# Optimization experiments

Hardware: AMD Instinct MI355X
Metric: run time of the kernel (lower is better)

The kernel has to match this reference:

```python
import jax, jax.numpy as jnp
import numpy as np


def setup_inputs() -> dict:
    key = jax.random.key(0)
    k1, k2 = jax.random.split(key)
    a_bar = jax.random.normal(k1, (32, 512, 512), dtype=jnp.float32)
    b_bar = jax.random.normal(k2, (32, 512, 512), dtype=jnp.float32)
    return {"a_bar": a_bar, "b_bar": b_bar}


def reference(a_bar, b_bar):
    # e[b,i,j] = <a_bar[b,i,:], b_bar[b,j,:]>
    e = jnp.einsum("bid,bjd->bij", a_bar, b_bar)
    # a_tilde: row softmax (over j) then weighted sum of b rows
    attn_a = jax.nn.softmax(e, axis=2)            # [B, Sa, Sb]
    a_tilde = jnp.einsum("bij,bjd->bid", attn_a, b_bar)
    # b_tilde: column softmax (over i), transposed, times a_bar
    attn_b = jax.nn.softmax(e, axis=1)            # [B, Sa, Sb]
    b_tilde = jnp.einsum("bij,bid->bjd", attn_b, a_bar)
    m_a = jnp.concatenate([a_bar, a_tilde, a_bar - a_tilde, a_bar * a_tilde], axis=-1)
    m_b = jnp.concatenate([b_bar, b_tilde, b_bar - b_tilde, b_bar * b_tilde], axis=-1)
    return (m_a, m_b)
```

## Files before the change

### kernel.cpp

```cpp
#include <hip/hip_runtime.h>
#include <hip/hip_bf16.h>
#include <math.h>

#define B_   32
#define S_   512
#define SxS  (S_ * S_)
#define LOG2E 1.4426950408889634f

using frag_ab = __attribute__((ext_vector_type(8))) short;
using frag_cd = __attribute__((ext_vector_type(4))) float;

__device__ inline short f2bf(float x) {
    __hip_bfloat16 h = __float2bfloat16(x);
    return *reinterpret_cast<short*>(&h);
}
__device__ inline float bf2f(short s) {
    __hip_bfloat16 h = *reinterpret_cast<__hip_bfloat16*>(&s);
    return __bfloat162float(h);
}
__device__ __forceinline__ int swz(int r) { return (r ^ (r >> 3)) & 7; }

__device__ __forceinline__ void async16(const short* g, short* l) {
    __builtin_amdgcn_global_load_lds(
        (const __attribute__((address_space(1))) void*)g,
        (__attribute__((address_space(3))) void*)l,
        16, 0, 0);
}

__global__ __launch_bounds__(256) void k_prep(const float* __restrict__ A,
                                              const float* __restrict__ Bm,
                                              short* __restrict__ PA,
                                              short* __restrict__ PB,
                                              short* __restrict__ Va,
                                              short* __restrict__ Vb)
{
    const int z   = blockIdx.z;
    const int b   = z & 31;
    const int isB = z >> 5;
    const float* X = (isB ? Bm : A) + (size_t)b * SxS;
    short* P  = (isB ? PB : PA) + (size_t)b * (S_ * 1024);
    short* Vp = (isB ? Vb : Va) + (size_t)b * SxS;
    const float scale = isB ? 1.0f : LOG2E;

    const int i0 = blockIdx.y * 64, d0 = blockIdx.x * 64;

    __shared__ short T[64][72];

    const int sl = threadIdx.x & 7;
    const int il = threadIdx.x >> 3;

    #pragma unroll
    for (int p = 0; p < 2; ++p) {
        const int i    = il + 32 * p;
        const int rowg = i0 + i;
        const float* src = X + (size_t)rowg * S_ + d0 + sl * 8;
        const float4 v0 = *(const float4*)(src);
        const float4 v1 = *(const float4*)(src + 4);

        T[sl * 8 + 0][i] = f2bf(v0.x); T[sl * 8 + 1][i] = f2bf(v0.y);
        T[sl * 8 + 2][i] = f2bf(v0.z); T[sl * 8 + 3][i] = f2bf(v0.w);
        T[sl * 8 + 4][i] = f2bf(v1.x); T[sl * 8 + 5][i] = f2bf(v1.y);
        T[sl * 8 + 6][i] = f2bf(v1.z); T[sl * 8 + 7][i] = f2bf(v1.w);

        const float xs[8] = {v0.x, v0.y, v0.z, v0.w, v1.x, v1.y, v1.z, v1.w};
        frag_ab hi, lo;
        #pragma unroll
        for (int j = 0; j < 8; ++j) {
            const float x = xs[j] * scale;
            const short h = f2bf(x);
            hi[j] = h;
            lo[j] = f2bf(x - bf2f(h));
        }
        const int W = (d0 >> 5) + (sl >> 2);
        const int q = sl & 3;
        short* base = P + (size_t)rowg * 1024 + W * 64;
        *(frag_ab*)(base + (((2 * q)     ^ (rowg & 7)) * 8)) = hi;
        *(frag_ab*)(base + (((2 * q + 1) ^ (rowg & 7)) * 8)) = lo;
    }
    __syncthreads();

    const int pc = threadIdx.x & 7, dl = threadIdx.x >> 3;
    #pragma unroll
    for (int p = 0; p < 2; ++p) {
        const int d  = dl + 32 * p;
        const int dg = d0 + d;
        frag_ab t = *(const frag_ab*)&T[d][pc * 8];
        *(frag_ab*)(Vp + (size_t)dg * 512 + i0 + ((pc ^ (dg & 7)) * 8)) = t;
    }
}

__global__ __launch_bounds__(256) void k_gemm_e(const short* __restrict__ PA,
                                                const short* __restrict__ PB,
                                                float* __restrict__ E)
{
    const int lin     = blockIdx.x + (blockIdx.y << 2) + (blockIdx.z << 4);
    const int logical = ((lin & 7) << 6) + (lin >> 3);
    const int b  = logical >> 4;
    const int i0 = ((logical >> 2) & 3) * 128;
    const int j0 = (logical & 3) * 128;

    const short* Ab = PA + (size_t)b * (S_ * 1024);
    const short* Bb = PB + (size_t)b * (S_ * 1024);
    float* Eb = E + (size_t)b * SxS;

    __shared__ __align__(16) short As[128][64];
    __shared__ __align__(16) short Bs[128][64];

    const int tid  = threadIdx.x;
    const int wave = tid >> 6, lane = tid & 63;
    const int wr   = wave >> 1, wc = wave & 1;
    const int q    = lane >> 4, m = lane & 15;
    const int srow = lane >> 3, schunk = lane & 7;

    frag_cd zero = {0.f, 0.f, 0.f, 0.f};
    frag_cd acc[4][4];
    #pragma unroll
    for (int i = 0; i < 4; ++i)
        #pragma unroll
        for (int j = 0; j < 4; ++j) acc[i][j] = zero;

    for (int k0 = 0; k0 < S_; k0 += 32) {
        const int W = k0 >> 5;
        __syncthreads();
        #pragma unroll
        for (int p = 0; p < 4; ++p) {
            const int seg    = wave * 4 + p;
            const int rowg_a = i0 + seg * 8 + srow;
            const int rowg_b = j0 + seg * 8 + srow;
            async16(Ab + (size_t)rowg_a * 1024 + W * 64 + schunk * 8, &As[seg * 8][0]);
            async16(Bb + (size_t)rowg_b * 1024 + W * 64 + schunk * 8, &Bs[seg * 8][0]);
        }
        __syncthreads();

        frag_ab ah[4], al[4], bh[4], bl[4];
        #pragma unroll
        for (int t = 0; t < 4; ++t) {
            const int ra = wr * 64 + t * 16 + m;
            const int rb = wc * 64 + t * 16 + m;
            ah[t] = *(const frag_ab*)&As[ra][((2 * q)     ^ (ra & 7)) * 8];
            al[t] = *(const frag_ab*)&As[ra][((2 * q + 1) ^ (ra & 7)) * 8];
            bh[t] = *(const frag_ab*)&Bs[rb][((2 * q)     ^ (rb & 7)) * 8];
            bl[t] = *(const frag_ab*)&Bs[rb][((2 * q + 1) ^ (rb & 7)) * 8];
        }
        #pragma unroll
        for (int mt = 0; mt < 4; ++mt)
            #pragma unroll
            for (int nt = 0; nt < 4; ++nt) {
                acc[mt][nt] = __builtin_amdgcn_mfma_f32_16x16x32_bf16(ah[mt], bh[nt], acc[mt][nt], 0, 0, 0);
                acc[mt][nt] = __builtin_amdgcn_mfma_f32_16x16x32_bf16(ah[mt], bl[nt], acc[mt][nt], 0, 0, 0);
                acc[mt][nt] = __builtin_amdgcn_mfma_f32_16x16x32_bf16(al[mt], bh[nt], acc[mt][nt], 0, 0, 0);
            }
    }

    #pragma unroll
    for (int mt = 0; mt < 4; ++mt)
        #pragma unroll
        for (int nt = 0; nt < 4; ++nt) {
            const int rb  = i0 + wr * 64 + mt * 16 + q * 4;
            const int col = j0 + wc * 64 + nt * 16 + m;
            Eb[(size_t)(rb + 0) * S_ + col] = acc[mt][nt][0];
            Eb[(size_t)(rb + 1) * S_ + col] = acc[mt][nt][1];
            Eb[(size_t)(rb + 2) * S_ + col] = acc[mt][nt][2];
            Eb[(size_t)(rb + 3) * S_ + col] = acc[mt][nt][3];
        }
}

__global__ __launch_bounds__(256) void k_rstats(const float* __restrict__ E,
                                                float* __restrict__ rmax,
                                                float* __restrict__ rinv)
{
    const int row  = blockIdx.x * 4 + (threadIdx.x >> 6);
    const int lane = threadIdx.x & 63;
    const float* er = E + (size_t)row * S_;

    float4 v0 = *(const float4*)(er + lane * 4);
    float4 v1 = *(const float4*)(er + 256 + lane * 4);

    float m = fmaxf(fmaxf(fmaxf(v0.x, v0.y), fmaxf(v0.z, v0.w)),
                    fmaxf(fmaxf(v1.x, v1.y), fmaxf(v1.z, v1.w)));
    #pragma unroll
    for (int off = 32; off >= 1; off >>= 1)
        m = fmaxf(m, __shfl_xor(m, off));

    float s = exp2f(v0.x - m) + exp2f(v0.y - m)
            + exp2f(v0.z - m) + exp2f(v0.w - m)
            + exp2f(v1.x - m) + exp2f(v1.y - m)
            + exp2f(v1.z - m) + exp2f(v1.w - m);
    #pragma unroll
    for (int off = 32; off >= 1; off >>= 1)
        s += __shfl_xor(s, off);

    if (lane == 0) { rmax[row] = m; rinv[row] = 1.0f / s; }
}

__global__ __launch_bounds__(256) void k_cstats(const float* __restrict__ E,
                                                float* __restrict__ cmax,
                                                float* __restrict__ cinv)
{
    const int b  = blockIdx.x >> 3;
    const int s0 = (blockIdx.x & 7) * 64;
    const float* Eb = E + (size_t)b * SxS;

    __shared__ float scr[32][64];
    __shared__ float mS[64];

    const int tid = threadIdx.x;
    const int ib  = tid >> 3;
    const int sub = tid & 7;

    float pm[8];
    #pragma unroll
    for (int c = 0; c < 8; ++c) pm[c] = -INFINITY;
    for (int ii = 0; ii < 16; ++ii) {
        const float* p = Eb + (size_t)(ib * 16 + ii) * S_ + s0 + sub * 8;
        const float4 u  = *(const float4*)p;
        const float4 u2 = *(const float4*)(p + 4);
        pm[0] = fmaxf(pm[0], u.x);  pm[1] = fmaxf(pm[1], u.y);
        pm[2] = fmaxf(pm[2], u.z);  pm[3] = fmaxf(pm[3], u.w);
        pm[4] = fmaxf(pm[4], u2.x); pm[5] = fmaxf(pm[5], u2.y);
        pm[6] = fmaxf(pm[6], u2.z); pm[7] = fmaxf(pm[7], u2.w);
    }
    #pragma unroll
    for (int c = 0; c < 8; ++c) scr[ib][sub * 8 + c] = pm[c];
    __syncthreads();
    if (tid < 64) {
        float v = scr[0][tid];
        #pragma unroll
        for (int k = 1; k < 32; ++k) v = fmaxf(v, scr[k][tid]);
        mS[tid] = v;
        cmax[b * S_ + s0 + tid] = v;
    }
    __syncthreads();

    float ps[8];
    #pragma unroll
    for (int c = 0; c < 8; ++c) ps[c] = 0.f;
    for (int ii = 0; ii < 16; ++ii) {
        const float* p = Eb + (size_t)(ib * 16 + ii) * S_ + s0 + sub * 8;
        const float4 u  = *(const float4*)p;
        const float4 u2 = *(const float4*)(p + 4);
        const float xs[8] = {u.x, u.y, u.z, u.w, u2.x, u2.y, u2.z, u2.w};
        #pragma unroll
        for (int c = 0; c < 8; ++c) ps[c] += exp2f(xs[c] - mS[sub * 8 + c]);
    }
    __syncthreads();
    #pragma unroll
    for (int c = 0; c < 8; ++c) scr[ib][sub * 8 + c] = ps[c];
    __syncthreads();
    if (tid < 64) {
        float v = 0.f;
        #pragma unroll
        for (int k = 0; k < 32; ++k) v += scr[k][tid];
        cinv[b * S_ + s0 + tid] = 1.0f / v;
    }
}

__global__ __launch_bounds__(256) void k_pv(const float* __restrict__ E,
                                            const float* __restrict__ rmx_,
                                            const float* __restrict__ rin_,
                                            const float* __restrict__ cmx_,
                                            const float* __restrict__ cin_,
                                            const short* __restrict__ Va,
                                            const short* __restrict__ Vb,
                                            const float* __restrict__ A,
                                            const float* __restrict__ Bm,
                                            float* __restrict__ Ma,
                                            float* __restrict__ Mb)
{
    const int lin = blockIdx.x;
    const int wg  = ((lin & 7) << 8) | (lin >> 3);
    const int side = wg >> 10;
    const int b    = (wg >> 5) & 31;
    const int rs   = (wg >> 1) & 15;
    const int dh   = wg & 1;
    const int s0   = rs * 32;

    const float* Eb  = E + (size_t)b * SxS;
    const float* pmx = (side ? cmx_ : rmx_) + b * S_;
    const float* piv = (side ? cin_ : rin_) + b * S_;
    const short* Vg  = (side ? Va : Vb) + (size_t)b * SxS;
    const float* Xb  = (side ? Bm : A) + (size_t)b * SxS;
    float* Ob = (side ? Mb : Ma) + (size_t)b * S_ * 2048;

    __shared__ __align__(16) short Pl[32][512];
    __shared__ __align__(16) short Vs[256][64];
    __shared__ float riS[32];

    const int tid = threadIdx.x;
    const int wv  = tid >> 6, lane = tid & 63;
    const int q   = lane >> 4, m = lane & 15;

    if (tid < 32) riS[tid] = piv[s0 + tid];

    if (side == 0) {
        const int rl = tid >> 3, sub = tid & 7;
        const float mx = pmx[s0 + rl];
        const float* er = Eb + (size_t)(s0 + rl) * S_;
        const int sl = (sub ^ swz(rl)) * 8;
        #pragma unroll
        for (int fi = 0; fi < 8; ++fi) {
            const float* p = er + sub * 8 + fi * 64;
            const float4 u  = *(const float4*)p;
            const float4 u2 = *(const float4*)(p + 4);
            const float xs[8] = {u.x, u.y, u.z, u.w, u2.x, u2.y, u2.z, u2.w};
            frag_ab pb;
            #pragma unroll
            for (int j = 0; j < 8; ++j) pb[j] = f2bf(exp2f(xs[j] - mx));
            *(frag_ab*)&Pl[rl][fi * 64 + sl] = pb;
        }
    } else {
        const int ib = tid >> 2, cs = tid & 3;
        float mloc[8];
        #pragma unroll
        for (int c = 0; c < 8; ++c) mloc[c] = pmx[s0 + cs * 8 + c];
        frag_ab pb[8];
        #pragma unroll
        for (int ii = 0; ii < 8; ++ii) {
            const float* p = Eb + (size_t)(ib * 8 + ii) * S_ + s0 + cs * 8;
            const float4 u  = *(const float4*)p;
            const float4 u2 = *(const float4*)(p + 4);
            const float xs[8] = {u.x, u.y, u.z, u.w, u2.x, u2.y, u2.z, u2.w};
            #pragma unroll
            for (int c = 0; c < 8; ++c)
                pb[c][ii] = f2bf(exp2f(xs[c] - mloc[c]));
        }
        #pragma unroll
        for (int c = 0; c < 8; ++c) {
            const int cl = cs * 8 + c;
            *(frag_ab*)&Pl[cl][((ib ^ swz(cl)) & 63) * 8
                               + (ib & ~7) * 0] = pb[c];
        }
    }

    frag_cd zero = {0.f, 0.f, 0.f, 0.f};
    frag_cd acc[2][4];
    #pragma unroll
    for (int i = 0; i < 2; ++i)
        #pragma unroll
        for (int j = 0; j < 4; ++j) acc[i][j] = zero;

    for (int k0 = 0; k0 < S_; k0 += 64) {
        __syncthreads();
        #pragma unroll
        for (int p = 0; p < 8; ++p) {
            const int seg = p * 32 + wv * 8;
            const int d   = dh * 256 + seg + (lane >> 3);
            async16(Vg + (size_t)d * 512 + k0 + (lane & 7) * 8, &Vs[seg][0]);
        }
        __syncthreads();

        #pragma unroll
        for (int kk = 0; kk < 2; ++kk) {
            frag_ab af[2], bf[4];
            #pragma unroll
            for (int t = 0; t < 2; ++t) {
                const int ra = t * 16 + m;
                af[t] = *(const frag_ab*)&Pl[ra][k0 + (((kk * 4 + q) ^ swz(ra)) * 8)];
            }
            #pragma unroll
            for (int t = 0; t < 4; ++t) {
                const int dl = wv * 64 + t * 16 + m;
                bf[t] = *(const frag_ab*)&Vs[dl][(((kk * 4 + q) ^ (dl & 7)) * 8)];
            }
            #pragma unroll
            for (int mt = 0; mt < 2; ++mt)
                #pragma unroll
                for (int nt = 0; nt < 4; ++nt)
                    acc[mt][nt] = __builtin_amdgcn_mfma_f32_16x16x32_bf16(af[mt], bf[nt], acc[mt][nt], 0, 0, 0);
        }
    }

    #pragma unroll
    for (int mt = 0; mt < 2; ++mt)
        #pragma unroll
        for (int nt = 0; nt < 4; ++nt) {
            const int colg = dh * 256 + wv * 64 + nt * 16 + m;
            #pragma unroll
            for (int rr = 0; rr < 4; ++rr) {
                const int rl   = mt * 16 + q * 4 + rr;
                const int rowg = s0 + rl;
                const float at = acc[mt][nt][rr] * riS[rl];
                const float xv = Xb[(size_t)rowg * S_ + colg];
                float* o = Ob + (size_t)rowg * 2048 + colg;
                o[0]    = xv;
                o[512]  = at;
                o[1024] = xv - at;
                o[1536] = xv * at;
            }
        }
}

extern "C" void kernel_launch(void* const* d_in, const int* in_sizes, int n_in,
                              void* d_out, int out_size, void* d_ws, size_t ws_size,
                              hipStream_t stream)
{
    const float* A  = (const float*)d_in[0];
    const float* Bm = (const float*)d_in[1];
    float* Ma = (float*)d_out;
    float* Mb = Ma + (size_t)B_ * S_ * 2048;

    float* E    = (float*)d_ws;
    short* Va   = (short*)(E + (size_t)B_ * SxS);
    short* Vb   = Va + (size_t)B_ * SxS;
    float* rmax = (float*)(Vb + (size_t)B_ * SxS);
    float* rinv = rmax + B_ * S_;
    float* cmax = rinv + B_ * S_;
    float* cinv = cmax + B_ * S_;

    short* PA = (short*)d_out;
    short* PB = PA + (size_t)B_ * S_ * 1024;

    k_prep  <<<dim3(8, 8, 64),    256, 0, stream>>>(A, Bm, PA, PB, Va, Vb);
    k_gemm_e<<<dim3(4, 4, 32),    256, 0, stream>>>(PA, PB, E);
    k_rstats<<<dim3(B_ * S_ / 4), 256, 0, stream>>>(E, rmax, rinv);
    k_cstats<<<dim3(B_ * 8),      256, 0, stream>>>(E, cmax, cinv);
    k_pv    <<<dim3(2048),        256, 0, stream>>>(E, rmax, rinv, cmax, cinv,
                                                    Va, Vb, A, Bm, Ma, Mb);
}
```

Baseline: 475.7 us.

## Fuse five-kernel pipeline into one cooperative persistent kernel with grid syncs

Replaces the five separate launches (prep, E GEMM, row stats, column stats, PV) with a single cooperative kernel of 256 persistent blocks that loops over the original work items and separates the phases with grid.sync(). The aim is to remove per-launch overhead and inter-kernel gaps. The cost is that each phase now runs on only 256 workgroups with about 64KB of shared memory each, which lowers occupancy and parallelism, especially in the E GEMM phase, which has only 512 tiles. If the cooperative launch fails, it falls back to the old launches.

Result: slower. 615.5 us (+29.4%).

```diff
diff --git a/kernel.cpp b/kernel.cpp
--- a/kernel.cpp
+++ b/kernel.cpp
@@ -1,6 +1,9 @@
 #include <hip/hip_runtime.h>
+#include <hip/hip_cooperative_groups.h>
 #include <hip/hip_bf16.h>
 #include <math.h>
+
+namespace cg = cooperative_groups;
 
 #define B_   32
 #define S_   512
@@ -25,6 +28,371 @@
         (const __attribute__((address_space(1))) void*)g,
         (__attribute__((address_space(3))) void*)l,
         16, 0, 0);
+}
+
+__global__ __launch_bounds__(256) void k_mega(const float* __restrict__ A,
+                                              const float* __restrict__ Bm,
+                                              short* __restrict__ PA,
+                                              short* __restrict__ PB,
+                                              short* __restrict__ Va,
+                                              short* __restrict__ Vb,
+                                              float* __restrict__ E,
+                                              float* __restrict__ rmax,
+                                              float* __restrict__ rinv,
+                                              float* __restrict__ cmax,
+                                              float* __restrict__ cinv,
+                                              float* __restrict__ Ma,
+                                              float* __restrict__ Mb)
+{
+    cg::grid_group grid = cg::this_grid();
+    const int pb  = blockIdx.x;
+    const int tid = threadIdx.x;
+
+    __shared__ __align__(16) char smem[65792];
+
+    {
+        short (*T)[72] = (short(*)[72])smem;
+        const int sl = tid & 7;
+        const int il = tid >> 3;
+        const int pc = tid & 7, dl = tid >> 3;
+
+        for (int lin = pb; lin < 4096; lin += 256) {
+            __syncthreads();
+            const int bx = lin & 7, by = (lin >> 3) & 7, z = lin >> 6;
+            const int b   = z & 31;
+            const int isB = z >> 5;
+            const float* X = (isB ? Bm : A) + (size_t)b * SxS;
+            short* P  = (isB ? PB : PA) + (size_t)b * (S_ * 1024);
+            short* Vp = (isB ? Vb : Va) + (size_t)b * SxS;
+            const float scale = isB ? 1.0f : LOG2E;
+            const int i0 = by * 64, d0 = bx * 64;
+
+            #pragma unroll
+            for (int pp = 0; pp < 2; ++pp) {
+                const int i    = il + 32 * pp;
+                const int rowg = i0 + i;
+                const float* src = X + (size_t)rowg * S_ + d0 + sl * 8;
+                const float4 v0 = *(const float4*)(src);
+                const float4 v1 = *(const float4*)(src + 4);
+
+                T[sl * 8 + 0][i] = f2bf(v0.x); T[sl * 8 + 1][i] = f2bf(v0.y);
+                T[sl * 8 + 2][i] = f2bf(v0.z); T[sl * 8 + 3][i] = f2bf(v0.w);
+                T[sl * 8 + 4][i] = f2bf(v1.x); T[sl * 8 + 5][i] = f2bf(v1.y);
+                T[sl * 8 + 6][i] = f2bf(v1.z); T[sl * 8 + 7][i] = f2bf(v1.w);
+
+                const float xs[8] = {v0.x, v0.y, v0.z, v0.w, v1.x, v1.y, v1.z, v1.w};
+                frag_ab hi, lo;
+                #pragma unroll
+                for (int j = 0; j < 8; ++j) {
+                    const float x = xs[j] * scale;
+                    const short h = f2bf(x);
+                    hi[j] = h;
+                    lo[j] = f2bf(x - bf2f(h));
+                }
+                const int W = (d0 >> 5) + (sl >> 2);
+                const int q = sl & 3;
+                short* base = P + (size_t)rowg * 1024 + W * 64;
+                *(frag_ab*)(base + (((2 * q)     ^ (rowg & 7)) * 8)) = hi;
+                *(frag_ab*)(base + (((2 * q + 1) ^ (rowg & 7)) * 8)) = lo;
+            }
+            __syncthreads();
+
+            #pragma unroll
+            for (int pp = 0; pp < 2; ++pp) {
+                const int d  = dl + 32 * pp;
+                const int dg = d0 + d;
+                frag_ab t = *(const frag_ab*)&T[d][pc * 8];
+                *(frag_ab*)(Vp + (size_t)dg * 512 + i0 + ((pc ^ (dg & 7)) * 8)) = t;
+            }
+        }
+    }
+    __syncthreads();
+    grid.sync();
+
+    {
+        short (*As)[64] = (short(*)[64])smem;
+        short (*Bs)[64] = (short(*)[64])(smem + 16384);
+
+        const int wave = tid >> 6, lane = tid & 63;
+        const int wr   = wave >> 1, wc = wave & 1;
+        const int q    = lane >> 4, m = lane & 15;
+        const int srow = lane >> 3, schunk = lane & 7;
+
+        for (int lin = pb; lin < 512; lin += 256) {
+            const int logical = ((lin & 7) << 6) + (lin >> 3);
+            const int b  = logical >> 4;
+            const int i0 = ((logical >> 2) & 3) * 128;
+            const int j0 = (logical & 3) * 128;
+
+            const short* Ab = PA + (size_t)b * (S_ * 1024);
+            const short* Bb = PB + (size_t)b * (S_ * 1024);
+            float* Eb = E + (size_t)b * SxS;
+
+            frag_cd zero = {0.f, 0.f, 0.f, 0.f};
+            frag_cd acc[4][4];
+            #pragma unroll
+            for (int i = 0; i < 4; ++i)
+                #pragma unroll
+                for (int j = 0; j < 4; ++j) acc[i][j] = zero;
+
+            for (int k0 = 0; k0 < S_; k0 += 32) {
+                const int W = k0 >> 5;
+                __syncthreads();
+                #pragma unroll
+                for (int p = 0; p < 4; ++p) {
+                    const int seg    = wave * 4 + p;
+                    const int rowg_a = i0 + seg * 8 + srow;
+                    const int rowg_b = j0 + seg * 8 + srow;
+                    async16(Ab + (size_t)rowg_a * 1024 + W * 64 + schunk * 8, &As[seg * 8][0]);
+                    async16(Bb + (size_t)rowg_b * 1024 + W * 64 + schunk * 8, &Bs[seg * 8][0]);
+                }
+                __syncthreads();
+
+                frag_ab ah[4], al[4], bh[4], bl[4];
+                #pragma unroll
+                for (int t = 0; t < 4; ++t) {
+                    const int ra = wr * 64 + t * 16 + m;
+                    const int rb = wc * 64 + t * 16 + m;
+                    ah[t] = *(const frag_ab*)&As[ra][((2 * q)     ^ (ra & 7)) * 8];
+                    al[t] = *(const frag_ab*)&As[ra][((2 * q + 1) ^ (ra & 7)) * 8];
+                    bh[t] = *(const frag_ab*)&Bs[rb][((2 * q)     ^ (rb & 7)) * 8];
+                    bl[t] = *(const frag_ab*)&Bs[rb][((2 * q + 1) ^ (rb & 7)) * 8];
+                }
+                #pragma unroll
+                for (int mt = 0; mt < 4; ++mt)
+                    #pragma unroll
+                    for (int nt = 0; nt < 4; ++nt) {
+                        acc[mt][nt] = __builtin_amdgcn_mfma_f32_16x16x32_bf16(ah[mt], bh[nt], acc[mt][nt], 0, 0, 0);
+                        acc[mt][nt] = __builtin_amdgcn_mfma_f32_16x16x32_bf16(ah[mt], bl[nt], acc[mt][nt], 0, 0, 0);
+                        acc[mt][nt] = __builtin_amdgcn_mfma_f32_16x16x32_bf16(al[mt], bh[nt], acc[mt][nt], 0, 0, 0);
+                    }
+            }
+
+            #pragma unroll
+            for (int mt = 0; mt < 4; ++mt)
+                #pragma unroll
+                for (int nt = 0; nt < 4; ++nt) {
+                    const int rb  = i0 + wr * 64 + mt * 16 + q * 4;
+                    const int col = j0 + wc * 64 + nt * 16 + m;
+                    Eb[(size_t)(rb + 0) * S_ + col] = acc[mt][nt][0];
+                    Eb[(size_t)(rb + 1) * S_ + col] = acc[mt][nt][1];
+                    Eb[(size_t)(rb + 2) * S_ + col] = acc[mt][nt][2];
+                    Eb[(size_t)(rb + 3) * S_ + col] = acc[mt][nt][3];
+                }
+            __syncthreads();
+        }
+    }
+    grid.sync();
+
+    {
+        const int lane = tid & 63;
+        for (int lin = pb; lin < 4096; lin += 256) {
+            const int row = lin * 4 + (tid >> 6);
+            const float* er = E + (size_t)row * S_;
+
+            float4 v0 = *(const float4*)(er + lane * 4);
+            float4 v1 = *(const float4*)(er + 256 + lane * 4);
+
+            float m = fmaxf(fmaxf(fmaxf(v0.x, v0.y), fmaxf(v0.z, v0.w)),
+                            fmaxf(fmaxf(v1.x, v1.y), fmaxf(v1.z, v1.w)));
+            #pragma unroll
+            for (int off = 32; off >= 1; off >>= 1)
+                m = fmaxf(m, __shfl_xor(m, off));
+
+            float s = exp2f(v0.x - m) + exp2f(v0.y - m)
+                    + exp2f(v0.z - m) + exp2f(v0.w - m)
+                    + exp2f(v1.x - m) + exp2f(v1.y - m)
+                    + exp2f(v1.z - m) + exp2f(v1.w - m);
+            #pragma unroll
+            for (int off = 32; off >= 1; off >>= 1)
+                s += __shfl_xor(s, off);
+
+            if (lane == 0) { rmax[row] = m; rinv[row] = 1.0f / s; }
+        }
+
+        float (*scr)[64] = (float(*)[64])smem;
+        float* mS = (float*)(smem + 8192);
+
+        const int b  = pb >> 3;
+        const int s0 = (pb & 7) * 64;
+        const float* Eb = E + (size_t)b * SxS;
+
+        const int ib  = tid >> 3;
+        const int sub = tid & 7;
+
+        __syncthreads();
+        float pm[8];
+        #pragma unroll
+        for (int c = 0; c < 8; ++c) pm[c] = -INFINITY;
+        for (int ii = 0; ii < 16; ++ii) {
+            const float* p = Eb + (size_t)(ib * 16 + ii) * S_ + s0 + sub * 8;
+            const float4 u  = *(const float4*)p;
+            const float4 u2 = *(const float4*)(p + 4);
+            pm[0] = fmaxf(pm[0], u.x);  pm[1] = fmaxf(pm[1], u.y);
+            pm[2] = fmaxf(pm[2], u.z);  pm[3] = fmaxf(pm[3], u.w);
+            pm[4] = fmaxf(pm[4], u2.x); pm[5] = fmaxf(pm[5], u2.y);
+            pm[6] = fmaxf(pm[6], u2.z); pm[7] = fmaxf(pm[7], u2.w);
+        }
+        #pragma unroll
+        for (int c = 0; c < 8; ++c) scr[ib][sub * 8 + c] = pm[c];
+        __syncthreads();
+        if (tid < 64) {
+            float v = scr[0][tid];
+            #pragma unroll
+            for (int k = 1; k < 32; ++k) v = fmaxf(v, scr[k][tid]);
+            mS[tid] = v;
+            cmax[b * S_ + s0 + tid] = v;
+        }
+        __syncthreads();
+
+        float ps[8];
+        #pragma unroll
+        for (int c = 0; c < 8; ++c) ps[c] = 0.f;
+        for (int ii = 0; ii < 16; ++ii) {
+            const float* p = Eb + (size_t)(ib * 16 + ii) * S_ + s0 + sub * 8;
+            const float4 u  = *(const float4*)p;
+            const float4 u2 = *(const float4*)(p + 4);
+            const float xs[8] = {u.x, u.y, u.z, u.w, u2.x, u2.y, u2.z, u2.w};
+            #pragma unroll
+            for (int c = 0; c < 8; ++c) ps[c] += exp2f(xs[c] - mS[sub * 8 + c]);
+        }
+        __syncthreads();
+        #pragma unroll
+        for (int c = 0; c < 8; ++c) scr[ib][sub * 8 + c] = ps[c];
+        __syncthreads();
+        if (tid < 64) {
+            float v = 0.f;
+            #pragma unroll
+            for (int k = 0; k < 32; ++k) v += scr[k][tid];
+            cinv[b * S_ + s0 + tid] = 1.0f / v;
+        }
+        __syncthreads();
+    }
+    grid.sync();
+
+    {
+        short (*Pl)[512] = (short(*)[512])smem;
+        short (*Vs)[64]  = (short(*)[64])(smem + 32768);
+        float* riS       = (float*)(smem + 65536);
+
+        const int wv = tid >> 6, lane = tid & 63;
+        const int q  = lane >> 4, m = lane & 15;
+
+        for (int lin = pb; lin < 2048; lin += 256) {
+            __syncthreads();
+            const int wg   = ((lin & 7) << 8) | (lin >> 3);
+            const int side = wg >> 10;
+            const int b    = (wg >> 5) & 31;
+            const int rs   = (wg >> 1) & 15;
+            const int dh   = wg & 1;
+            const int s0   = rs * 32;
+
+            const float* Eb  = E + (size_t)b * SxS;
+            const float* pmx = (side ? cmax : rmax) + b * S_;
+            const float* piv = (side ? cinv : rinv) + b * S_;
+            const short* Vg  = (side ? Va : Vb) + (size_t)b * SxS;
+            const float* Xb  = (side ? Bm : A) + (size_t)b * SxS;
+            float* Ob = (side ? Mb : Ma) + (size_t)b * S_ * 2048;
+
+            if (tid < 32) riS[tid] = piv[s0 + tid];
+
+            if (side == 0) {
+                const int rl = tid >> 3, sub = tid & 7;
+                const float mx = pmx[s0 + rl];
+                const float* er = Eb + (size_t)(s0 + rl) * S_;
+                const int sl = (sub ^ swz(rl)) * 8;
+                #pragma unroll
+                for (int fi = 0; fi < 8; ++fi) {
+                    const float* p = er + sub * 8 + fi * 64;
+                    const float4 u  = *(const float4*)p;
+                    const float4 u2 = *(const float4*)(p + 4);
+                    const float xs[8] = {u.x, u.y, u.z, u.w, u2.x, u2.y, u2.z, u2.w};
+                    frag_ab pbf;
+                    #pragma unroll
+                    for (int j = 0; j < 8; ++j) pbf[j] = f2bf(exp2f(xs[j] - mx));
+                    *(frag_ab*)&Pl[rl][fi * 64 + sl] = pbf;
+                }
+            } else {
+                const int ib = tid >> 2, cs = tid & 3;
+                float mloc[8];
+                #pragma unroll
+                for (int c = 0; c < 8; ++c) mloc[c] = pmx[s0 + cs * 8 + c];
+                frag_ab pbf[8];
+                #pragma unroll
+                for (int ii = 0; ii < 8; ++ii) {
+                    const float* p = Eb + (size_t)(ib * 8 + ii) * S_ + s0 + cs * 8;
+                    const float4 u  = *(const float4*)p;
+                    const float4 u2 = *(const float4*)(p + 4);
+                    const float xs[8] = {u.x, u.y, u.z, u.w, u2.x, u2.y, u2.z, u2.w};
+                    #pragma unroll
+                    for (int c = 0; c < 8; ++c)
+                        pbf[c][ii] = f2bf(exp2f(xs[c] - mloc[c]));
+                }
+                #pragma unroll
+                for (int c = 0; c < 8; ++c) {
+                    const int cl = cs * 8 + c;
+                    *(frag_ab*)&Pl[cl][((ib ^ swz(cl)) & 63) * 8] = pbf[c];
+                }
+            }
+
+            frag_cd zero = {0.f, 0.f, 0.f, 0.f};
+            frag_cd acc[2][4];
+            #pragma unroll
+            for (int i = 0; i < 2; ++i)
+                #pragma unroll
+                for (int j = 0; j < 4; ++j) acc[i][j] = zero;
+
+            for (int k0 = 0; k0 < S_; k0 += 64) {
+                __syncthreads();
+                #pragma unroll
+                for (int p = 0; p < 8; ++p) {
+                    const int seg = p * 32 + wv * 8;
+                    const int d   = dh * 256 + seg + (lane >> 3);
+                    async16(Vg + (size_t)d * 512 + k0 + (lane & 7) * 8, &Vs[seg][0]);
+                }
+                __syncthreads();
+
+                #pragma unroll
+                for (int kk = 0; kk < 2; ++kk) {
+                    frag_ab af[2], bf[4];
+                    #pragma unroll
+                    for (int t = 0; t < 2; ++t) {
+                        const int ra = t * 16 + m;
+                        af[t] = *(const frag_ab*)&Pl[ra][k0 + (((kk * 4 + q) ^ swz(ra)) * 8)];
+                    }
+                    #pragma unroll
+                    for (int t = 0; t < 4; ++t) {
+                        const int dl = wv * 64 + t * 16 + m;
+                        bf[t] = *(const frag_ab*)&Vs[dl][(((kk * 4 + q) ^ (dl & 7)) * 8)];
+                    }
+                    #pragma unroll
+                    for (int mt = 0; mt < 2; ++mt)
+                        #pragma unroll
+                        for (int nt = 0; nt < 4; ++nt)
+                            acc[mt][nt] = __builtin_amdgcn_mfma_f32_16x16x32_bf16(af[mt], bf[nt], acc[mt][nt], 0, 0, 0);
+                }
+            }
+
+            #pragma unroll
+            for (int mt = 0; mt < 2; ++mt)
+                #pragma unroll
+                for (int nt = 0; nt < 4; ++nt) {
+                    const int colg = dh * 256 + wv * 64 + nt * 16 + m;
+                    #pragma unroll
+                    for (int rr = 0; rr < 4; ++rr) {
+                        const int rl   = mt * 16 + q * 4 + rr;
+                        const int rowg = s0 + rl;
+                        const float at = acc[mt][nt][rr] * riS[rl];
+                        const float xv = Xb[(size_t)rowg * S_ + colg];
+                        float* o = Ob + (size_t)rowg * 2048 + colg;
+                        o[0]    = xv;
+                        o[512]  = at;
+                        o[1024] = xv - at;
+                        o[1536] = xv * at;
+                    }
+                }
+        }
+    }
 }
 
 __global__ __launch_bounds__(256) void k_prep(const float* __restrict__ A,
@@ -327,8 +695,7 @@
         #pragma unroll
         for (int c = 0; c < 8; ++c) {
             const int cl = cs * 8 + c;
-            *(frag_ab*)&Pl[cl][((ib ^ swz(cl)) & 63) * 8
-                               + (ib & ~7) * 0] = pb[c];
+            *(frag_ab*)&Pl[cl][((ib ^ swz(cl)) & 63) * 8] = pb[c];
         }
     }
 
@@ -410,10 +777,19 @@
     short* PA = (short*)d_out;
     short* PB = PA + (size_t)B_ * S_ * 1024;
 
-    k_prep  <<<dim3(8, 8, 64),    256, 0, stream>>>(A, Bm, PA, PB, Va, Vb);
-    k_gemm_e<<<dim3(4, 4, 32),    256, 0, stream>>>(PA, PB, E);
-    k_rstats<<<dim3(B_ * S_ / 4), 256, 0, stream>>>(E, rmax, rinv);
-    k_cstats<<<dim3(B_ * 8),      256, 0, stream>>>(E, cmax, cinv);
-    k_pv    <<<dim3(2048),        256, 0, stream>>>(E, rmax, rinv, cmax, cinv,
-                                                    Va, Vb, A, Bm, Ma, Mb);
-}
+    void* args[] = {
+        (void*)&A, (void*)&Bm, (void*)&PA, (void*)&PB, (void*)&Va, (void*)&Vb,
+        (void*)&E, (void*)&rmax, (void*)&rinv, (void*)&cmax, (void*)&cinv,
+        (void*)&Ma, (void*)&Mb
+    };
+    hipError_t err = hipLaunchCooperativeKernel((void*)k_mega, dim3(256),
+                                                dim3(256), args, 0, stream);
+    if (err != hipSuccess) {
+        k_prep  <<<dim3(8, 8, 64),    256, 0, stream>>>(A, Bm, PA, PB, Va, Vb);
+        k_gemm_e<<<dim3(4, 4, 32),    256, 0, stream>>>(PA, PB, E);
+        k_rstats<<<dim3(B_ * S_ / 4), 256, 0, stream>>>(E, rmax, rinv);
+        k_cstats<<<dim3(B_ * 8),      256, 0, stream>>>(E, cmax, cinv);
+        k_pv    <<<dim3(2048),        256, 0, stream>>>(E, rmax, rinv, cmax, cinv,
+                                                        Va, Vb, A, Bm, Ma, Mb);
+    }
+}
```

## Load MFMA operands directly from global memory, drop LDS staging in GEMMs

Applied to the files above, without the earlier changes.

Both the E GEMM and the P·V GEMM stop staging operand tiles through LDS via async global-to-LDS loads and per-iteration barriers. Each lane now reads its pre-swizzled 16-byte fragments straight from global memory (relying on L1/L2), keeping only the P tile in LDS for the second kernel. This removes two __syncthreads per k-step and the LDS write/read round trip. In exchange, data shared across waves is fetched redundantly from cache, which may raise global/L2 traffic and exposed latency without prefetching.

Result: slower. 512.6 us (+7.7%).

```diff
diff --git a/kernel.cpp b/kernel.cpp
--- a/kernel.cpp
+++ b/kernel.cpp
@@ -19,13 +19,6 @@
     return __bfloat162float(h);
 }
 __device__ __forceinline__ int swz(int r) { return (r ^ (r >> 3)) & 7; }
-
-__device__ __forceinline__ void async16(const short* g, short* l) {
-    __builtin_amdgcn_global_load_lds(
-        (const __attribute__((address_space(1))) void*)g,
-        (__attribute__((address_space(3))) void*)l,
-        16, 0, 0);
-}
 
 __global__ __launch_bounds__(256) void k_prep(const float* __restrict__ A,
                                               const float* __restrict__ Bm,
@@ -103,14 +96,21 @@
     const short* Bb = PB + (size_t)b * (S_ * 1024);
     float* Eb = E + (size_t)b * SxS;
 
-    __shared__ __align__(16) short As[128][64];
-    __shared__ __align__(16) short Bs[128][64];
-
     const int tid  = threadIdx.x;
     const int wave = tid >> 6, lane = tid & 63;
     const int wr   = wave >> 1, wc = wave & 1;
     const int q    = lane >> 4, m = lane & 15;
-    const int srow = lane >> 3, schunk = lane & 7;
+    const int mx7  = m & 7;
+    const int chi  = ((2 * q)     ^ mx7) * 8;
+    const int clo  = ((2 * q + 1) ^ mx7) * 8;
+
+    const short* arow[4];
+    const short* brow[4];
+    #pragma unroll
+    for (int t = 0; t < 4; ++t) {
+        arow[t] = Ab + (size_t)(i0 + wr * 64 + t * 16 + m) * 1024;
+        brow[t] = Bb + (size_t)(j0 + wc * 64 + t * 16 + m) * 1024;
+    }
 
     frag_cd zero = {0.f, 0.f, 0.f, 0.f};
     frag_cd acc[4][4];
@@ -120,27 +120,14 @@
         for (int j = 0; j < 4; ++j) acc[i][j] = zero;
 
     for (int k0 = 0; k0 < S_; k0 += 32) {
-        const int W = k0 >> 5;
-        __syncthreads();
-        #pragma unroll
-        for (int p = 0; p < 4; ++p) {
-            const int seg    = wave * 4 + p;
-            const int rowg_a = i0 + seg * 8 + srow;
-            const int rowg_b = j0 + seg * 8 + srow;
-            async16(Ab + (size_t)rowg_a * 1024 + W * 64 + schunk * 8, &As[seg * 8][0]);
-            async16(Bb + (size_t)rowg_b * 1024 + W * 64 + schunk * 8, &Bs[seg * 8][0]);
-        }
-        __syncthreads();
-
+        const int off = (k0 >> 5) * 64;
         frag_ab ah[4], al[4], bh[4], bl[4];
         #pragma unroll
         for (int t = 0; t < 4; ++t) {
-            const int ra = wr * 64 + t * 16 + m;
-            const int rb = wc * 64 + t * 16 + m;
-            ah[t] = *(const frag_ab*)&As[ra][((2 * q)     ^ (ra & 7)) * 8];
-            al[t] = *(const frag_ab*)&As[ra][((2 * q + 1) ^ (ra & 7)) * 8];
-            bh[t] = *(const frag_ab*)&Bs[rb][((2 * q)     ^ (rb & 7)) * 8];
-            bl[t] = *(const frag_ab*)&Bs[rb][((2 * q + 1) ^ (rb & 7)) * 8];
+            ah[t] = *(const frag_ab*)(arow[t] + off + chi);
+            al[t] = *(const frag_ab*)(arow[t] + off + clo);
+            bh[t] = *(const frag_ab*)(brow[t] + off + chi);
+            bl[t] = *(const frag_ab*)(brow[t] + off + clo);
         }
         #pragma unroll
         for (int mt = 0; mt < 4; ++mt)
@@ -283,12 +270,12 @@
     float* Ob = (side ? Mb : Ma) + (size_t)b * S_ * 2048;
 
     __shared__ __align__(16) short Pl[32][512];
-    __shared__ __align__(16) short Vs[256][64];
     __shared__ float riS[32];
 
     const int tid = threadIdx.x;
     const int wv  = tid >> 6, lane = tid & 63;
     const int q   = lane >> 4, m = lane & 15;
+    const int mx7 = m & 7;
 
     if (tid < 32) riS[tid] = piv[s0 + tid];
 
@@ -327,10 +314,19 @@
         #pragma unroll
         for (int c = 0; c < 8; ++c) {
             const int cl = cs * 8 + c;
-            *(frag_ab*)&Pl[cl][((ib ^ swz(cl)) & 63) * 8
-                               + (ib & ~7) * 0] = pb[c];
-        }
-    }
+            *(frag_ab*)&Pl[cl][((ib ^ swz(cl)) & 63) * 8] = pb[c];
+        }
+    }
+    __syncthreads();
+
+    const short* vrow[4];
+    int psw[2];
+    #pragma unroll
+    for (int t = 0; t < 4; ++t)
+        vrow[t] = Vg + (size_t)(dh * 256 + wv * 64 + t * 16 + m) * 512;
+    #pragma unroll
+    for (int t = 0; t < 2; ++t)
+        psw[t] = swz(t * 16 + m);
 
     frag_cd zero = {0.f, 0.f, 0.f, 0.f};
     frag_cd acc[2][4];
@@ -340,28 +336,16 @@
         for (int j = 0; j < 4; ++j) acc[i][j] = zero;
 
     for (int k0 = 0; k0 < S_; k0 += 64) {
-        __syncthreads();
-        #pragma unroll
-        for (int p = 0; p < 8; ++p) {
-            const int seg = p * 32 + wv * 8;
-            const int d   = dh * 256 + seg + (lane >> 3);
-            async16(Vg + (size_t)d * 512 + k0 + (lane & 7) * 8, &Vs[seg][0]);
-        }
-        __syncthreads();
-
         #pragma unroll
         for (int kk = 0; kk < 2; ++kk) {
+            const int c = kk * 4 + q;
             frag_ab af[2], bf[4];
             #pragma unroll
-            for (int t = 0; t < 2; ++t) {
-                const int ra = t * 16 + m;
-                af[t] = *(const frag_ab*)&Pl[ra][k0 + (((kk * 4 + q) ^ swz(ra)) * 8)];
-            }
-            #pragma unroll
-            for (int t = 0; t < 4; ++t) {
-                const int dl = wv * 64 + t * 16 + m;
-                bf[t] = *(const frag_ab*)&Vs[dl][(((kk * 4 + q) ^ (dl & 7)) * 8)];
-            }
+            for (int t = 0; t < 2; ++t)
+                af[t] = *(const frag_ab*)&Pl[t * 16 + m][k0 + ((c ^ psw[t]) * 8)];
+            #pragma unroll
+            for (int t = 0; t < 4; ++t)
+                bf[t] = *(const frag_ab*)(vrow[t] + k0 + ((c ^ mx7) * 8));
             #pragma unroll
             for (int mt = 0; mt < 2; ++mt)
                 #pragma unroll
```
